# Kernel optimization log

Hardware: AMD Instinct MI355X
Metric: run time of the kernel (lower is better)

## Reference

```python
import jax, jax.numpy as jnp
import numpy as np

E = 8        # ensemble_size
S = 64       # state_dim
A = 16       # action_dim
H = 256      # hidden_dim
B = 16384    # batch


def setup_inputs() -> dict:
    key = jax.random.key(0)
    ks = jax.random.split(key, 9)
    sc = lambda fan_in: 1.0 / np.sqrt(fan_in)
    return {
        "state": jax.random.normal(ks[0], (B, S), dtype=jnp.float32),
        # stacked per-member weights (PyTorch Linear: y = x @ W^T + b; here stored as [in, out])
        "W1": jax.random.uniform(ks[1], (E, S, H), jnp.float32, -sc(S), sc(S)),
        "b1": jax.random.uniform(ks[2], (E, H), jnp.float32, -sc(S), sc(S)),
        "W2": jax.random.uniform(ks[3], (E, H, H), jnp.float32, -sc(H), sc(H)),
        "b2": jax.random.uniform(ks[4], (E, H), jnp.float32, -sc(H), sc(H)),
        "Wf": jax.random.uniform(ks[5], (E, H, S), jnp.float32, -sc(H), sc(H)),
        "bf": jax.random.uniform(ks[6], (E, S), jnp.float32, -sc(H), sc(H)),
        "Wg": jax.random.uniform(ks[7], (E, H, S * A), jnp.float32, -sc(H), sc(H)),
        "bg": jax.random.uniform(ks[8], (E, S * A), jnp.float32, -sc(H), sc(H)),
    }


def reference(state, W1, b1, W2, b2, Wf, bf, Wg, bg):
    # DynamicsEnsemble.forward(state, enable_dropout=False): dropout inactive in eval mode.
    # Batched over ensemble members via einsum (e=member, b=batch).
    h = jnp.tanh(jnp.einsum("bs,esh->ebh", state, W1) + b1[:, None, :])   # [E,B,H]
    h = jnp.tanh(jnp.einsum("ebh,ehk->ebk", h, W2) + b2[:, None, :])      # [E,B,H]
    f = jnp.einsum("ebh,ehs->ebs", h, Wf) + bf[:, None, :]                # [E,B,S]
    g = jnp.einsum("ebh,ehq->ebq", h, Wg) + bg[:, None, :]                # [E,B,S*A]
    f_mean = jnp.mean(f, axis=0)                                          # [B,S]
    g_mean = jnp.mean(g, axis=0).reshape(state.shape[0], S, A)            # [B,S,A]
    return f_mean, g_mean
```

## Files before the change

### kernel.cpp

```cpp
#include <hip/hip_runtime.h>
#include <stdint.h>


#define BSZ   16384
#define EDIM  8
#define SDIM  64
#define HDIM  256
#define NOUT  1088
#define NPAD  1152
#define KCAT  2048

typedef __attribute__((ext_vector_type(8))) short s16x8;
typedef __attribute__((ext_vector_type(4))) float f32x4;

__device__ __forceinline__ unsigned short f2bf(float x) {
  unsigned int u = __float_as_uint(x);
  u += 0x7fffu + ((u >> 16) & 1u);
  return (unsigned short)(u >> 16);
}

__device__ __forceinline__ float fast_tanh(float x) {
  float t = __expf(2.0f * x);
  return 1.0f - 2.0f / (t + 1.0f);
}

__device__ __forceinline__ void gload_lds16(const unsigned short* g, unsigned short* l) {
  __builtin_amdgcn_global_load_lds(
      (__attribute__((address_space(1))) void*)(g),
      (__attribute__((address_space(3))) void*)(l), 16, 0, 0);
}


__global__ void conv_state_kernel(const float* __restrict__ src,
                                  unsigned short* __restrict__ dst) {
  int i = (blockIdx.x * 256 + threadIdx.x) * 4;
  const float4 v = *reinterpret_cast<const float4*>(src + i);
  ushort4 o;
  o.x = f2bf(v.x); o.y = f2bf(v.y); o.z = f2bf(v.z); o.w = f2bf(v.w);
  *reinterpret_cast<ushort4*>(dst + i) = o;
}

__global__ void tr_f32_bf16_kernel(const float* __restrict__ src,
                                   unsigned short* __restrict__ dst,
                                   int R, int C, long sBatch, long dBatch, int dPitch) {
  __shared__ float t[32][33];
  src += (size_t)blockIdx.z * sBatch;
  dst += (size_t)blockIdx.z * dBatch;
  const int c0 = blockIdx.x * 32, r0 = blockIdx.y * 32;
  const int tx = threadIdx.x, ty = threadIdx.y;
  #pragma unroll
  for (int i = 0; i < 32; i += 8) {
    int r = r0 + ty + i;
    if (r < R && c0 + tx < C) t[ty + i][tx] = src[(size_t)r * C + c0 + tx];
  }
  __syncthreads();
  #pragma unroll
  for (int i = 0; i < 32; i += 8) {
    int c = c0 + ty + i;
    if (c < C && r0 + tx < R)
      dst[(size_t)c * dPitch + (r0 + tx)] = f2bf(t[tx][ty + i]);
  }
}

__global__ void bias_mean_kernel(const float* __restrict__ bf,
                                 const float* __restrict__ bg,
                                 float* __restrict__ bm) {
  int n = blockIdx.x * 256 + threadIdx.x;
  if (n >= NOUT) return;
  float s = 0.f;
  #pragma unroll
  for (int e = 0; e < EDIM; ++e)
    s += (n < SDIM) ? bf[e * SDIM + n] : bg[e * 1024 + (n - SDIM)];
  bm[n] = s * 0.125f;
}


template <int KK>
__global__ __launch_bounds__(256) void gemm_tanh_kernel(
    const unsigned short* __restrict__ Ab,
    const unsigned short* __restrict__ Bb,
    const float* __restrict__ biasb,
    unsigned short* __restrict__ houtb,
    long aStride) {
  __shared__ unsigned short As[2][4096];
  __shared__ unsigned short Bs[2][4096];
  const int tid = threadIdx.x;
  const int lane = tid & 63;
  const int wv = tid >> 6;
  const int wr = wv >> 1, wc = wv & 1;
  const int mtile = blockIdx.x * 128;
  const int ntile = blockIdx.y * 128;
  const int e = blockIdx.z;
  const unsigned short* Ag = Ab + (size_t)e * aStride;
  const unsigned short* Bg = Bb + (size_t)e * (HDIM * KK);
  const float* bias = biasb + e * HDIM;
  unsigned short* hout = houtb + (size_t)e * ((size_t)BSZ * HDIM);
  const int lr = lane & 15, lk = lane >> 4;

  f32x4 acc[4][4];
  #pragma unroll
  for (int i = 0; i < 4; ++i)
    #pragma unroll
    for (int j = 0; j < 4; ++j) acc[i][j] = (f32x4){0.f, 0.f, 0.f, 0.f};

  auto stage = [&](int buf, int kk) {
    #pragma unroll
    for (int i = 0; i < 2; ++i) {
      const int s0 = wv * 64 + i * 256;
      const int s = s0 + lane;
      const int row = s >> 2;
      const int w = s & 3;
      gload_lds16(Ag + (size_t)(mtile + row) * KK + (kk + w * 8), &As[buf][s0 * 8]);
      gload_lds16(Bg + (size_t)(ntile + row) * KK + (kk + w * 8), &Bs[buf][s0 * 8]);
    }
  };

  stage(0, 0);
  __syncthreads();
  constexpr int NSTEP = KK / 32;
  #pragma unroll
  for (int t = 0; t < NSTEP; ++t) {
    const int cur = t & 1;
    if (t + 1 < NSTEP) stage(cur ^ 1, (t + 1) * 32);
    s16x8 av[4], bv[4];
    #pragma unroll
    for (int mi = 0; mi < 4; ++mi)
      av[mi] = *(const s16x8*)&As[cur][(wr * 64 + mi * 16 + lr) * 32 + lk * 8];
    #pragma unroll
    for (int nj = 0; nj < 4; ++nj)
      bv[nj] = *(const s16x8*)&Bs[cur][(wc * 64 + nj * 16 + lr) * 32 + lk * 8];
    #pragma unroll
    for (int mi = 0; mi < 4; ++mi)
      #pragma unroll
      for (int nj = 0; nj < 4; ++nj)
        acc[mi][nj] = __builtin_amdgcn_mfma_f32_16x16x32_bf16(av[mi], bv[nj], acc[mi][nj], 0, 0, 0);
    __syncthreads();
  }

  #pragma unroll
  for (int nj = 0; nj < 4; ++nj) {
    const int col = ntile + wc * 64 + nj * 16 + lr;
    const float bc = bias[col];
    #pragma unroll
    for (int mi = 0; mi < 4; ++mi)
      #pragma unroll
      for (int r = 0; r < 4; ++r) {
        const int row = mtile + wr * 64 + mi * 16 + lk * 4 + r;
        hout[(size_t)row * HDIM + col] = f2bf(fast_tanh(acc[mi][nj][r] + bc));
      }
  }
}

__global__ __launch_bounds__(256) void gemm_out_kernel(
    const unsigned short* __restrict__ h2b,
    const unsigned short* __restrict__ Wcat,
    const float* __restrict__ bm,
    float* __restrict__ out) {
  __shared__ unsigned short As[2][4096];
  __shared__ unsigned short Bs[2][4096];
  const int tid = threadIdx.x;
  const int lane = tid & 63;
  const int wv = tid >> 6;
  const int wr = wv >> 1, wc = wv & 1;
  const int mtile = blockIdx.x * 128;
  const int ntile = blockIdx.y * 128;
  const int lr = lane & 15, lk = lane >> 4;

  f32x4 acc[4][4];
  #pragma unroll
  for (int i = 0; i < 4; ++i)
    #pragma unroll
    for (int j = 0; j < 4; ++j) acc[i][j] = (f32x4){0.f, 0.f, 0.f, 0.f};

  auto stage = [&](int buf, int kk) {
    const int e = kk >> 8;
    const int kl = kk & 255;
    #pragma unroll
    for (int i = 0; i < 2; ++i) {
      const int s0 = wv * 64 + i * 256;
      const int s = s0 + lane;
      const int row = s >> 2;
      const int w = s & 3;
      gload_lds16(h2b + ((size_t)e * BSZ + mtile + row) * HDIM + (kl + w * 8),
                  &As[buf][s0 * 8]);
      gload_lds16(Wcat + (size_t)(ntile + row) * KCAT + (kk + w * 8),
                  &Bs[buf][s0 * 8]);
    }
  };

  stage(0, 0);
  __syncthreads();
  constexpr int NSTEP = KCAT / 32;
  #pragma unroll 2
  for (int t = 0; t < NSTEP; ++t) {
    const int cur = t & 1;
    if (t + 1 < NSTEP) stage(cur ^ 1, (t + 1) * 32);
    s16x8 av[4], bv[4];
    #pragma unroll
    for (int mi = 0; mi < 4; ++mi)
      av[mi] = *(const s16x8*)&As[cur][(wr * 64 + mi * 16 + lr) * 32 + lk * 8];
    #pragma unroll
    for (int nj = 0; nj < 4; ++nj)
      bv[nj] = *(const s16x8*)&Bs[cur][(wc * 64 + nj * 16 + lr) * 32 + lk * 8];
    #pragma unroll
    for (int mi = 0; mi < 4; ++mi)
      #pragma unroll
      for (int nj = 0; nj < 4; ++nj)
        acc[mi][nj] = __builtin_amdgcn_mfma_f32_16x16x32_bf16(av[mi], bv[nj], acc[mi][nj], 0, 0, 0);
    __syncthreads();
  }

  #pragma unroll
  for (int nj = 0; nj < 4; ++nj) {
    const int col = ntile + wc * 64 + nj * 16 + lr;
    if (col < NOUT) {
      const float bc = bm[col];
      #pragma unroll
      for (int mi = 0; mi < 4; ++mi)
        #pragma unroll
        for (int r = 0; r < 4; ++r) {
          const int row = mtile + wr * 64 + mi * 16 + lk * 4 + r;
          const float v = acc[mi][nj][r] * 0.125f + bc;
          if (col < SDIM) out[(size_t)row * SDIM + col] = v;
          else out[(size_t)BSZ * SDIM + (size_t)row * 1024 + (col - SDIM)] = v;
        }
    }
  }
}


extern "C" void kernel_launch(void* const* d_in, const int* in_sizes, int n_in,
                              void* d_out, int out_size, void* d_ws, size_t ws_size,
                              hipStream_t stream) {
  (void)in_sizes; (void)n_in; (void)out_size;
  const float* state = (const float*)d_in[0];
  const float* W1 = (const float*)d_in[1];
  const float* b1 = (const float*)d_in[2];
  const float* W2 = (const float*)d_in[3];
  const float* b2 = (const float*)d_in[4];
  const float* Wf = (const float*)d_in[5];
  const float* bf = (const float*)d_in[6];
  const float* Wg = (const float*)d_in[7];
  const float* bg = (const float*)d_in[8];
  float* out = (float*)d_out;

  const size_t SZ_SB   = (size_t)BSZ * SDIM * 2;
  const size_t SZ_H    = (size_t)EDIM * BSZ * HDIM * 2;
  const size_t SZ_W1T  = (size_t)EDIM * HDIM * SDIM * 2;
  const size_t SZ_W2T  = (size_t)EDIM * HDIM * HDIM * 2;
  const size_t SZ_WCAT = (size_t)NPAD * KCAT * 2;
  const size_t SZ_BM   = (size_t)NOUT * 4;
  const size_t OFF_SB = 0;
  const size_t OFF_H1 = OFF_SB + SZ_SB;
  const size_t OFF_H2 = OFF_H1 + SZ_H;
  const size_t OFF_W1T = OFF_H2 + SZ_H;
  const size_t OFF_W2T = OFF_W1T + SZ_W1T;
  const size_t OFF_WCAT = OFF_W2T + SZ_W2T;
  const size_t OFF_BM = OFF_WCAT + SZ_WCAT;
  const size_t TOTAL = OFF_BM + SZ_BM;
  if (ws_size < TOTAL) return;

  char* ws = (char*)d_ws;
  unsigned short* sB   = (unsigned short*)(ws + OFF_SB);
  unsigned short* h1B  = (unsigned short*)(ws + OFF_H1);
  unsigned short* h2B  = (unsigned short*)(ws + OFF_H2);
  unsigned short* W1t  = (unsigned short*)(ws + OFF_W1T);
  unsigned short* W2t  = (unsigned short*)(ws + OFF_W2T);
  unsigned short* Wcat = (unsigned short*)(ws + OFF_WCAT);
  float* bm            = (float*)(ws + OFF_BM);

  hipMemsetAsync(Wcat, 0, SZ_WCAT, stream);
  conv_state_kernel<<<1024, 256, 0, stream>>>(state, sB);
  dim3 tb(32, 8);
  tr_f32_bf16_kernel<<<dim3(8, 2, 8), tb, 0, stream>>>(W1, W1t, 64, 256,
      (long)64 * 256, (long)256 * 64, 64);
  tr_f32_bf16_kernel<<<dim3(8, 8, 8), tb, 0, stream>>>(W2, W2t, 256, 256,
      65536L, 65536L, 256);
  tr_f32_bf16_kernel<<<dim3(2, 8, 8), tb, 0, stream>>>(Wf, Wcat, 256, 64,
      (long)256 * 64, 256L, KCAT);
  tr_f32_bf16_kernel<<<dim3(32, 8, 8), tb, 0, stream>>>(Wg, Wcat + 64 * KCAT, 256, 1024,
      (long)256 * 1024, 256L, KCAT);
  bias_mean_kernel<<<5, 256, 0, stream>>>(bf, bg, bm);

  gemm_tanh_kernel<64><<<dim3(128, 2, 8), 256, 0, stream>>>(sB, W1t, b1, h1B, 0L);
  gemm_tanh_kernel<256><<<dim3(128, 2, 8), 256, 0, stream>>>(h1B, W2t, b2, h2B,
      (long)BSZ * HDIM);
  gemm_out_kernel<<<dim3(128, 9), 256, 0, stream>>>(h2B, Wcat, bm, out);
}
```

Baseline: 288.5 us.

## Swizzle LDS slots, widen output GEMM N-tile to 192, remap blocks per XCD

Applies an XOR swizzle to the LDS k-slot layout in both GEMM kernels so the MFMA operand reads avoid bank conflicts, and raises wave priority around the MFMA loop. The output GEMM moves from 128x128 to 128x192 tiles (6 N-tiles covering 1152) and launches a 1D grid of 768 blocks. Blocks are remapped so consecutive blocks on each XCD share M tiles, which should improve cache reuse. The larger accumulator tile raises register use, and launch_bounds(256,3) may force spills.

Result: faster. 265.6 us (-7.9%).

```diff
diff --git a/kernel.cpp b/kernel.cpp
--- a/kernel.cpp
+++ b/kernel.cpp
@@ -29,6 +29,8 @@
       (__attribute__((address_space(1))) void*)(g),
       (__attribute__((address_space(3))) void*)(l), 16, 0, 0);
 }
+
+__device__ __forceinline__ int swz_slot(int row, int sl) { return sl ^ ((row >> 1) & 3); }
 
 
 __global__ void conv_state_kernel(const float* __restrict__ src,
@@ -109,9 +111,9 @@
       const int s0 = wv * 64 + i * 256;
       const int s = s0 + lane;
       const int row = s >> 2;
-      const int w = s & 3;
-      gload_lds16(Ag + (size_t)(mtile + row) * KK + (kk + w * 8), &As[buf][s0 * 8]);
-      gload_lds16(Bg + (size_t)(ntile + row) * KK + (kk + w * 8), &Bs[buf][s0 * 8]);
+      const int kap = swz_slot(row, s & 3);
+      gload_lds16(Ag + (size_t)(mtile + row) * KK + (kk + kap * 8), &As[buf][s0 * 8]);
+      gload_lds16(Bg + (size_t)(ntile + row) * KK + (kk + kap * 8), &Bs[buf][s0 * 8]);
     }
   };
 
@@ -124,16 +126,22 @@
     if (t + 1 < NSTEP) stage(cur ^ 1, (t + 1) * 32);
     s16x8 av[4], bv[4];
     #pragma unroll
-    for (int mi = 0; mi < 4; ++mi)
-      av[mi] = *(const s16x8*)&As[cur][(wr * 64 + mi * 16 + lr) * 32 + lk * 8];
-    #pragma unroll
-    for (int nj = 0; nj < 4; ++nj)
-      bv[nj] = *(const s16x8*)&Bs[cur][(wc * 64 + nj * 16 + lr) * 32 + lk * 8];
+    for (int mi = 0; mi < 4; ++mi) {
+      const int r = wr * 64 + mi * 16 + lr;
+      av[mi] = *(const s16x8*)&As[cur][r * 32 + swz_slot(r, lk) * 8];
+    }
+    #pragma unroll
+    for (int nj = 0; nj < 4; ++nj) {
+      const int r = wc * 64 + nj * 16 + lr;
+      bv[nj] = *(const s16x8*)&Bs[cur][r * 32 + swz_slot(r, lk) * 8];
+    }
+    __builtin_amdgcn_s_setprio(1);
     #pragma unroll
     for (int mi = 0; mi < 4; ++mi)
       #pragma unroll
       for (int nj = 0; nj < 4; ++nj)
         acc[mi][nj] = __builtin_amdgcn_mfma_f32_16x16x32_bf16(av[mi], bv[nj], acc[mi][nj], 0, 0, 0);
+    __builtin_amdgcn_s_setprio(0);
     __syncthreads();
   }
 
@@ -151,26 +159,27 @@
   }
 }
 
-__global__ __launch_bounds__(256) void gemm_out_kernel(
+__global__ __launch_bounds__(256, 3) void gemm_out_kernel(
     const unsigned short* __restrict__ h2b,
     const unsigned short* __restrict__ Wcat,
     const float* __restrict__ bm,
     float* __restrict__ out) {
   __shared__ unsigned short As[2][4096];
-  __shared__ unsigned short Bs[2][4096];
+  __shared__ unsigned short Bs[2][6144];
   const int tid = threadIdx.x;
   const int lane = tid & 63;
   const int wv = tid >> 6;
   const int wr = wv >> 1, wc = wv & 1;
-  const int mtile = blockIdx.x * 128;
-  const int ntile = blockIdx.y * 128;
+  const int logical = (blockIdx.x & 7) * 96 + (blockIdx.x >> 3);
+  const int mtile = (logical / 6) * 128;
+  const int ntile = (logical % 6) * 192;
   const int lr = lane & 15, lk = lane >> 4;
 
-  f32x4 acc[4][4];
+  f32x4 acc[4][6];
   #pragma unroll
   for (int i = 0; i < 4; ++i)
     #pragma unroll
-    for (int j = 0; j < 4; ++j) acc[i][j] = (f32x4){0.f, 0.f, 0.f, 0.f};
+    for (int j = 0; j < 6; ++j) acc[i][j] = (f32x4){0.f, 0.f, 0.f, 0.f};
 
   auto stage = [&](int buf, int kk) {
     const int e = kk >> 8;
@@ -180,10 +189,17 @@
       const int s0 = wv * 64 + i * 256;
       const int s = s0 + lane;
       const int row = s >> 2;
-      const int w = s & 3;
-      gload_lds16(h2b + ((size_t)e * BSZ + mtile + row) * HDIM + (kl + w * 8),
+      const int kap = swz_slot(row, s & 3);
+      gload_lds16(h2b + ((size_t)e * BSZ + mtile + row) * HDIM + (kl + kap * 8),
                   &As[buf][s0 * 8]);
-      gload_lds16(Wcat + (size_t)(ntile + row) * KCAT + (kk + w * 8),
+    }
+    #pragma unroll
+    for (int i = 0; i < 3; ++i) {
+      const int s0 = wv * 64 + i * 256;
+      const int s = s0 + lane;
+      const int row = s >> 2;
+      const int kap = swz_slot(row, s & 3);
+      gload_lds16(Wcat + (size_t)(ntile + row) * KCAT + (kk + kap * 8),
                   &Bs[buf][s0 * 8]);
     }
   };
@@ -195,24 +211,30 @@
   for (int t = 0; t < NSTEP; ++t) {
     const int cur = t & 1;
     if (t + 1 < NSTEP) stage(cur ^ 1, (t + 1) * 32);
-    s16x8 av[4], bv[4];
-    #pragma unroll
-    for (int mi = 0; mi < 4; ++mi)
-      av[mi] = *(const s16x8*)&As[cur][(wr * 64 + mi * 16 + lr) * 32 + lk * 8];
-    #pragma unroll
-    for (int nj = 0; nj < 4; ++nj)
-      bv[nj] = *(const s16x8*)&Bs[cur][(wc * 64 + nj * 16 + lr) * 32 + lk * 8];
+    s16x8 av[4], bv[6];
+    #pragma unroll
+    for (int mi = 0; mi < 4; ++mi) {
+      const int r = wr * 64 + mi * 16 + lr;
+      av[mi] = *(const s16x8*)&As[cur][r * 32 + swz_slot(r, lk) * 8];
+    }
+    #pragma unroll
+    for (int nj = 0; nj < 6; ++nj) {
+      const int r = wc * 96 + nj * 16 + lr;
+      bv[nj] = *(const s16x8*)&Bs[cur][r * 32 + swz_slot(r, lk) * 8];
+    }
+    __builtin_amdgcn_s_setprio(1);
     #pragma unroll
     for (int mi = 0; mi < 4; ++mi)
       #pragma unroll
-      for (int nj = 0; nj < 4; ++nj)
+      for (int nj = 0; nj < 6; ++nj)
         acc[mi][nj] = __builtin_amdgcn_mfma_f32_16x16x32_bf16(av[mi], bv[nj], acc[mi][nj], 0, 0, 0);
+    __builtin_amdgcn_s_setprio(0);
     __syncthreads();
   }
 
   #pragma unroll
-  for (int nj = 0; nj < 4; ++nj) {
-    const int col = ntile + wc * 64 + nj * 16 + lr;
+  for (int nj = 0; nj < 6; ++nj) {
+    const int col = ntile + wc * 96 + nj * 16 + lr;
     if (col < NOUT) {
       const float bc = bm[col];
       #pragma unroll
@@ -285,5 +307,5 @@
   gemm_tanh_kernel<64><<<dim3(128, 2, 8), 256, 0, stream>>>(sB, W1t, b1, h1B, 0L);
   gemm_tanh_kernel<256><<<dim3(128, 2, 8), 256, 0, stream>>>(h1B, W2t, b2, h2B,
       (long)BSZ * HDIM);
-  gemm_out_kernel<<<dim3(128, 9), 256, 0, stream>>>(h2B, Wcat, bm, out);
-}
+  gemm_out_kernel<<<768, 256, 0, stream>>>(h2B, Wcat, bm, out);
+}
```
